# Kernel optimization log

Measured on AMD Instinct MI355X. Metric: run time of the kernel, lower is better.

Reference implementation:

```python
import jax, jax.numpy as jnp
import numpy as np

N = 100000   # nodes
D = 128      # in_ft == out_ft (residual mix requires equality)
E = 1600000  # edges (nnz of sparse A)


def setup_inputs() -> dict:
    key = jax.random.key(0)
    ks = jax.random.split(key, 8)
    X = jax.random.normal(ks[0], (N, D), dtype=jnp.float32)   # unused by forward math, kept for fidelity
    X0 = jax.random.normal(ks[1], (N, D), dtype=jnp.float32)
    row = jnp.sort(jax.random.randint(ks[2], (E,), 0, N))      # sparse A row indices (sorted)
    col = jax.random.randint(ks[3], (E,), 0, N)                # sparse A col indices
    vals = jax.random.uniform(ks[4], (E,), dtype=jnp.float32)  # sparse A values
    # nn.Linear(D, D): weight [out, in], bias [out]
    bound = 1.0 / np.sqrt(D)
    W = jax.random.uniform(ks[5], (D, D), minval=-bound, maxval=bound, dtype=jnp.float32)
    b = jax.random.uniform(ks[6], (D,), minval=-bound, maxval=bound, dtype=jnp.float32)
    alpha = jax.random.uniform(ks[7], (), dtype=jnp.float32)
    beta = jax.random.uniform(jax.random.fold_in(key, 7), (), dtype=jnp.float32)
    return {"X": X, "X0": X0, "row": row, "col": col, "vals": vals,
            "W": W, "b": b, "alpha": alpha, "beta": beta}


def reference(X, X0, row, col, vals, W, b, alpha, beta):
    # SpMM: (A @ X0)[i] = sum_e vals[e] * X0[col[e]] for edges with row[e] == i
    AX0 = jax.ops.segment_sum(vals[:, None] * X0[col], row, num_segments=N)  # [N, D]
    Xi = (1.0 - alpha) * AX0 + alpha * X0
    out = (1.0 - beta) * Xi + beta * (Xi @ W.T + b)
    return out
```

## Files before the change

### kernel.cpp

```cpp
#include <hip/hip_runtime.h>

#define D_FT 128

__device__ inline unsigned f2bf(float f) {
    unsigned u = __float_as_uint(f);
    return (u + 0x7FFFu + ((u >> 16) & 1u)) >> 16;
}
__device__ inline unsigned pack2bf(float a, float b) {
    return f2bf(a) | (f2bf(b) << 16);
}

typedef __attribute__((ext_vector_type(4))) float f32x4;
typedef __attribute__((ext_vector_type(8))) short bf16x8;

union bf8u { bf16x8 v; unsigned u[4]; };

__global__ __launch_bounds__(256) void build_row_ptr_kernel(
    const int* __restrict__ row, int* __restrict__ ptr, int n_edges, int n_nodes)
{
    const int e = blockIdx.x * 256 + threadIdx.x;
    if (e > n_edges) return;
    const int lo = (e == 0) ? 0 : row[e - 1] + 1;
    const int hi = (e == n_edges) ? n_nodes : row[e];
    for (int i = lo; i <= hi; ++i) ptr[i] = e;
}

template<bool USE_PTR>
__global__ __launch_bounds__(256) void spmm_mix_kernel(
    const float* __restrict__ X0,
    const int*   __restrict__ row,
    const int*   __restrict__ col,
    const float* __restrict__ vals,
    const int*   __restrict__ row_ptr,
    const float* __restrict__ alpha_p,
    float*       __restrict__ Xi,
    int n_nodes, int n_edges)
{
    const int wave = threadIdx.x >> 6;
    const int lane = threadIdx.x & 63;
    const int node = blockIdx.x * 4 + wave;
    if (node >= n_nodes) return;

    int ebeg, eend;
    if (USE_PTR) {
        ebeg = row_ptr[node];
        eend = row_ptr[node + 1];
    } else {
        int lo0 = 0, hi0 = n_edges, lo1 = 0, hi1 = n_edges;
        while ((lo0 < hi0) || (lo1 < hi1)) {
            int m0 = (lo0 + hi0) >> 1; if (m0 >= n_edges) m0 = n_edges - 1;
            int m1 = (lo1 + hi1) >> 1; if (m1 >= n_edges) m1 = n_edges - 1;
            const int r0v = row[m0];
            const int r1v = row[m1];
            if (lo0 < hi0) { if (r0v < node)     lo0 = m0 + 1; else hi0 = m0; }
            if (lo1 < hi1) { if (r1v < node + 1) lo1 = m1 + 1; else hi1 = m1; }
        }
        ebeg = lo0; eend = lo1;
    }

    const int d0 = lane * 2;
    float ax = 0.f, ay = 0.f;

    for (int e = ebeg; e < eend; e += 64) {
        const int n = min(64, eend - e);
        int   cl = 0; float vl = 0.f;
        if (lane < n) { cl = col[e + lane]; vl = vals[e + lane]; }
        for (int j0 = 0; j0 < n; j0 += 16) {
            float2 xs[16]; float vv[16];
            #pragma unroll
            for (int j = 0; j < 16; ++j) {
                const int c = __shfl(cl, j0 + j);
                vv[j] = __shfl(vl, j0 + j);
                xs[j] = *(const float2*)(X0 + (size_t)c * D_FT + d0);
            }
            #pragma unroll
            for (int j = 0; j < 16; ++j) {
                ax += vv[j] * xs[j].x;
                ay += vv[j] * xs[j].y;
            }
        }
    }

    const float alpha = *alpha_p;
    const float2 x0self = *(const float2*)(X0 + (size_t)node * D_FT + d0);
    float2 xi;
    xi.x = (1.f - alpha) * ax + alpha * x0self.x;
    xi.y = (1.f - alpha) * ay + alpha * x0self.y;
    *(float2*)(Xi + (size_t)node * D_FT + d0) = xi;
}

__global__ __launch_bounds__(256) void gemm_mix_kernel(
    const float* __restrict__ W,
    const float* __restrict__ bias,
    const float* __restrict__ beta_p,
    float*       __restrict__ io,
    int n_nodes)
{
    __shared__ __align__(16) char lds_raw[32768];
    char*  __restrict__ ldsB = lds_raw;
    float* __restrict__ ldsS = (float*)lds_raw;

    const int t   = threadIdx.x;
    const int w   = t >> 6;
    const int l   = t & 63;
    const int lhi = l >> 4;
    const int llo = l & 15;
    const int r0  = blockIdx.x * 64;

    int arow = r0 + w * 16 + llo;
    if (arow >= n_nodes) arow = n_nodes - 1;
    const float* aptr = io + (size_t)arow * D_FT;
    float4 af0[4], af1[4];
    #pragma unroll
    for (int ks = 0; ks < 4; ++ks) {
        const int k0 = ks * 32 + lhi * 8;
        af0[ks] = *(const float4*)(aptr + k0);
        af1[ks] = *(const float4*)(aptr + k0 + 4);
    }

    #pragma unroll
    for (int i = 0; i < 16; ++i) {
        const int f4 = i * 256 + t;
        const int o  = f4 >> 5;
        const int c4 = f4 & 31;
        const float4 x = *(const float4*)(W + (size_t)o * D_FT + c4 * 4);
        uint2 v; v.x = pack2bf(x.x, x.y); v.y = pack2bf(x.z, x.w);
        int byte = o * 256 + c4 * 8;
        byte ^= (o & 7) << 4;
        *(uint2*)(ldsB + byte) = v;
    }
    __syncthreads();

    f32x4 acc[8];
    #pragma unroll
    for (int n = 0; n < 8; ++n) acc[n] = (f32x4){0.f, 0.f, 0.f, 0.f};

    #pragma unroll
    for (int ks = 0; ks < 4; ++ks) {
        bf8u a;
        a.u[0] = pack2bf(af0[ks].x, af0[ks].y);
        a.u[1] = pack2bf(af0[ks].z, af0[ks].w);
        a.u[2] = pack2bf(af1[ks].x, af1[ks].y);
        a.u[3] = pack2bf(af1[ks].z, af1[ks].w);
        const int kb = ks * 64 + lhi * 16;
        #pragma unroll
        for (int n = 0; n < 8; ++n) {
            const int o = n * 16 + llo;
            int byte = o * 256 + kb;
            byte ^= (o & 7) << 4;
            const bf16x8 b = *(const bf16x8*)(ldsB + byte);
            acc[n] = __builtin_amdgcn_mfma_f32_16x16x32_bf16(a.v, b, acc[n], 0, 0, 0);
        }
    }

    __syncthreads();
    #pragma unroll
    for (int n = 0; n < 8; ++n) {
        const int C = n * 16 + llo;
        const int rt = w * 16 + lhi * 4;
        #pragma unroll
        for (int q = 0; q < 4; ++q)
            ldsS[(rt + q) * 128 + C] = acc[n][q];
    }
    __syncthreads();

    const float beta = *beta_p;
    const float ob = 1.f - beta;
    const int c4 = t & 31;
    const int rb = t >> 5;
    const float4 bb = *(const float4*)(bias + c4 * 4);

    #pragma unroll
    for (int i = 0; i < 8; ++i) {
        const int r  = rb * 8 + i;
        const int gr = r0 + r;
        if (gr < n_nodes) {
            const float4 a4  = *(const float4*)(ldsS + r * 128 + c4 * 4);
            const float4 xi4 = *(const float4*)(io + (size_t)gr * D_FT + c4 * 4);
            float4 o;
            o.x = ob * xi4.x + beta * (a4.x + bb.x);
            o.y = ob * xi4.y + beta * (a4.y + bb.y);
            o.z = ob * xi4.z + beta * (a4.z + bb.z);
            o.w = ob * xi4.w + beta * (a4.w + bb.w);
            *(float4*)(io + (size_t)gr * D_FT + c4 * 4) = o;
        }
    }
}

extern "C" void kernel_launch(void* const* d_in, const int* in_sizes, int n_in,
                              void* d_out, int out_size, void* d_ws, size_t ws_size,
                              hipStream_t stream) {
    const float* X0    = (const float*)d_in[1];
    const int*   row   = (const int*)  d_in[2];
    const int*   col   = (const int*)  d_in[3];
    const float* vals  = (const float*)d_in[4];
    const float* W     = (const float*)d_in[5];
    const float* b     = (const float*)d_in[6];
    const float* alpha = (const float*)d_in[7];
    const float* beta  = (const float*)d_in[8];
    float* out = (float*)d_out;

    const int n_nodes = in_sizes[1] / D_FT;
    const int n_edges = in_sizes[2];

    const size_t ptr_bytes = (size_t)(n_nodes + 1) * sizeof(int);
    const bool use_ptr = (ws_size >= ptr_bytes);

    if (use_ptr) {
        int* row_ptr = (int*)d_ws;
        build_row_ptr_kernel<<<(n_edges + 256) / 256, 256, 0, stream>>>(
            row, row_ptr, n_edges, n_nodes);
        spmm_mix_kernel<true><<<(n_nodes + 3) / 4, 256, 0, stream>>>(
            X0, row, col, vals, row_ptr, alpha, out, n_nodes, n_edges);
    } else {
        spmm_mix_kernel<false><<<(n_nodes + 3) / 4, 256, 0, stream>>>(
            X0, row, col, vals, nullptr, alpha, out, n_nodes, n_edges);
    }
    gemm_mix_kernel<<<(n_nodes + 63) / 64, 256, 0, stream>>>(
        W, b, beta, out, n_nodes);
}
```

Before: 274.9 us.

## Gather X0 in bf16 and pass bf16 intermediate from SpMM to GEMM

Adds a pre-pass that converts X0 to bf16 in workspace, so the SpMM gather reads 4 bytes per lane instead of 8 per edge row. The SpMM writes Xi as bf16 into workspace, and the GEMM reads the bf16 rows directly as MFMA A-fragments and writes fp32 output. This roughly halves the random-gather traffic and the intermediate traffic, at the cost of an extra conversion kernel and bf16 rounding of the aggregated features and of the residual term. Which path runs is selected by workspace size, with fp32 fallbacks kept.

```diff
diff --git a/kernel.cpp b/kernel.cpp
--- a/kernel.cpp
+++ b/kernel.cpp
@@ -9,11 +9,22 @@
 __device__ inline unsigned pack2bf(float a, float b) {
     return f2bf(a) | (f2bf(b) << 16);
 }
+__device__ inline float bf_lo(unsigned u) { return __uint_as_float(u << 16); }
+__device__ inline float bf_hi(unsigned u) { return __uint_as_float(u & 0xFFFF0000u); }
 
 typedef __attribute__((ext_vector_type(4))) float f32x4;
 typedef __attribute__((ext_vector_type(8))) short bf16x8;
 
-union bf8u { bf16x8 v; unsigned u[4]; };
+__global__ __launch_bounds__(256) void convert_x0_kernel(
+    const float* __restrict__ X0, unsigned* __restrict__ xb, int n4)
+{
+    const int i = blockIdx.x * 256 + threadIdx.x;
+    if (i < n4) {
+        const float4 x = ((const float4*)X0)[i];
+        uint2 v; v.x = pack2bf(x.x, x.y); v.y = pack2bf(x.z, x.w);
+        ((uint2*)xb)[i] = v;
+    }
+}
 
 __global__ __launch_bounds__(256) void build_row_ptr_kernel(
     const int* __restrict__ row, int* __restrict__ ptr, int n_edges, int n_nodes)
@@ -25,15 +36,17 @@
     for (int i = lo; i <= hi; ++i) ptr[i] = e;
 }
 
-template<bool USE_PTR>
+template<bool GB, bool XB, bool PTR>
 __global__ __launch_bounds__(256) void spmm_mix_kernel(
-    const float* __restrict__ X0,
-    const int*   __restrict__ row,
-    const int*   __restrict__ col,
-    const float* __restrict__ vals,
-    const int*   __restrict__ row_ptr,
-    const float* __restrict__ alpha_p,
-    float*       __restrict__ Xi,
+    const float*    __restrict__ X0,
+    const unsigned* __restrict__ X0b,
+    const int*      __restrict__ row,
+    const int*      __restrict__ col,
+    const float*    __restrict__ vals,
+    const int*      __restrict__ row_ptr,
+    const float*    __restrict__ alpha_p,
+    float*          __restrict__ Xi_f32,
+    unsigned*       __restrict__ Xi_bf,
     int n_nodes, int n_edges)
 {
     const int wave = threadIdx.x >> 6;
@@ -42,7 +55,7 @@
     if (node >= n_nodes) return;
 
     int ebeg, eend;
-    if (USE_PTR) {
+    if (PTR) {
         ebeg = row_ptr[node];
         eend = row_ptr[node + 1];
     } else {
@@ -66,17 +79,33 @@
         int   cl = 0; float vl = 0.f;
         if (lane < n) { cl = col[e + lane]; vl = vals[e + lane]; }
         for (int j0 = 0; j0 < n; j0 += 16) {
-            float2 xs[16]; float vv[16];
-            #pragma unroll
-            for (int j = 0; j < 16; ++j) {
-                const int c = __shfl(cl, j0 + j);
-                vv[j] = __shfl(vl, j0 + j);
-                xs[j] = *(const float2*)(X0 + (size_t)c * D_FT + d0);
-            }
-            #pragma unroll
-            for (int j = 0; j < 16; ++j) {
-                ax += vv[j] * xs[j].x;
-                ay += vv[j] * xs[j].y;
+            float vv[16];
+            if (GB) {
+                unsigned xs[16];
+                #pragma unroll
+                for (int j = 0; j < 16; ++j) {
+                    const int c = __shfl(cl, j0 + j);
+                    vv[j] = __shfl(vl, j0 + j);
+                    xs[j] = X0b[c * 64 + lane];
+                }
+                #pragma unroll
+                for (int j = 0; j < 16; ++j) {
+                    ax += vv[j] * bf_lo(xs[j]);
+                    ay += vv[j] * bf_hi(xs[j]);
+                }
+            } else {
+                float2 xs[16];
+                #pragma unroll
+                for (int j = 0; j < 16; ++j) {
+                    const int c = __shfl(cl, j0 + j);
+                    vv[j] = __shfl(vl, j0 + j);
+                    xs[j] = *(const float2*)(X0 + (size_t)c * D_FT + d0);
+                }
+                #pragma unroll
+                for (int j = 0; j < 16; ++j) {
+                    ax += vv[j] * xs[j].x;
+                    ay += vv[j] * xs[j].y;
+                }
             }
         }
     }
@@ -86,10 +115,107 @@
     float2 xi;
     xi.x = (1.f - alpha) * ax + alpha * x0self.x;
     xi.y = (1.f - alpha) * ay + alpha * x0self.y;
-    *(float2*)(Xi + (size_t)node * D_FT + d0) = xi;
-}
-
-__global__ __launch_bounds__(256) void gemm_mix_kernel(
+    if (XB) {
+        Xi_bf[node * 64 + lane] = pack2bf(xi.x, xi.y);
+    } else {
+        *(float2*)(Xi_f32 + (size_t)node * D_FT + d0) = xi;
+    }
+}
+
+__global__ __launch_bounds__(256) void gemm_mix_bf16_kernel(
+    const float*    __restrict__ W,
+    const float*    __restrict__ bias,
+    const float*    __restrict__ beta_p,
+    const unsigned* __restrict__ xi,
+    float*          __restrict__ out,
+    int n_nodes)
+{
+    __shared__ __align__(16) char lds_raw[32768];
+    char*  __restrict__ ldsB = lds_raw;
+    float* __restrict__ ldsS = (float*)lds_raw;
+
+    const int t   = threadIdx.x;
+    const int w   = t >> 6;
+    const int l   = t & 63;
+    const int lhi = l >> 4;
+    const int llo = l & 15;
+    const int r0  = blockIdx.x * 64;
+
+    int arow = r0 + w * 16 + llo;
+    if (arow >= n_nodes) arow = n_nodes - 1;
+    const char* aptr = (const char*)xi + (size_t)arow * 256;
+    bf16x8 a[4];
+    #pragma unroll
+    for (int ks = 0; ks < 4; ++ks)
+        a[ks] = *(const bf16x8*)(aptr + ks * 64 + lhi * 16);
+
+    #pragma unroll
+    for (int i = 0; i < 16; ++i) {
+        const int f4 = i * 256 + t;
+        const int o  = f4 >> 5;
+        const int c4 = f4 & 31;
+        const float4 x = *(const float4*)(W + (size_t)o * D_FT + c4 * 4);
+        uint2 v; v.x = pack2bf(x.x, x.y); v.y = pack2bf(x.z, x.w);
+        int byte = o * 256 + c4 * 8;
+        byte ^= (o & 7) << 4;
+        *(uint2*)(ldsB + byte) = v;
+    }
+    __syncthreads();
+
+    f32x4 acc[8];
+    #pragma unroll
+    for (int n = 0; n < 8; ++n) acc[n] = (f32x4){0.f, 0.f, 0.f, 0.f};
+
+    #pragma unroll
+    for (int ks = 0; ks < 4; ++ks) {
+        const int kb = ks * 64 + lhi * 16;
+        #pragma unroll
+        for (int n = 0; n < 8; ++n) {
+            const int o = n * 16 + llo;
+            int byte = o * 256 + kb;
+            byte ^= (o & 7) << 4;
+            const bf16x8 b = *(const bf16x8*)(ldsB + byte);
+            acc[n] = __builtin_amdgcn_mfma_f32_16x16x32_bf16(a[ks], b, acc[n], 0, 0, 0);
+        }
+    }
+
+    __syncthreads();
+    #pragma unroll
+    for (int n = 0; n < 8; ++n) {
+        const int C = n * 16 + llo;
+        const int rt = w * 16 + lhi * 4;
+        #pragma unroll
+        for (int q = 0; q < 4; ++q)
+            ldsS[(rt + q) * 128 + C] = acc[n][q];
+    }
+    __syncthreads();
+
+    const float beta = *beta_p;
+    const float ob = 1.f - beta;
+    const int c4 = t & 31;
+    const int rb = t >> 5;
+    const float4 bb = *(const float4*)(bias + c4 * 4);
+
+    #pragma unroll
+    for (int i = 0; i < 8; ++i) {
+        const int r  = rb * 8 + i;
+        const int gr = r0 + r;
+        if (gr < n_nodes) {
+            const float4 a4 = *(const float4*)(ldsS + r * 128 + c4 * 4);
+            const uint2  p  = ((const uint2*)(xi + (size_t)gr * 64))[c4];
+            float4 o;
+            o.x = ob * bf_lo(p.x) + beta * (a4.x + bb.x);
+            o.y = ob * bf_hi(p.x) + beta * (a4.y + bb.y);
+            o.z = ob * bf_lo(p.y) + beta * (a4.z + bb.z);
+            o.w = ob * bf_hi(p.y) + beta * (a4.w + bb.w);
+            *(float4*)(out + (size_t)gr * D_FT + c4 * 4) = o;
+        }
+    }
+}
+
+union bf8u { bf16x8 v; unsigned u[4]; };
+
+__global__ __launch_bounds__(256) void gemm_mix_f32_kernel(
     const float* __restrict__ W,
     const float* __restrict__ bias,
     const float* __restrict__ beta_p,
@@ -204,18 +330,47 @@
     const int n_edges = in_sizes[2];
 
     const size_t ptr_bytes = (size_t)(n_nodes + 1) * sizeof(int);
-    const bool use_ptr = (ws_size >= ptr_bytes);
-
-    if (use_ptr) {
-        int* row_ptr = (int*)d_ws;
+    const size_t BFOFF  = 524288;
+    const size_t BFSZ   = (size_t)n_nodes * 256;
+    const bool ptr_ok = (ws_size >= ptr_bytes);
+    const bool tierA  = ptr_ok && (ws_size >= BFOFF + 2 * BFSZ);
+    const bool tierAp = !tierA && ptr_ok && (ws_size >= BFOFF + BFSZ);
+
+    int* row_ptr = (int*)d_ws;
+    if (ptr_ok)
         build_row_ptr_kernel<<<(n_edges + 256) / 256, 256, 0, stream>>>(
             row, row_ptr, n_edges, n_nodes);
-        spmm_mix_kernel<true><<<(n_nodes + 3) / 4, 256, 0, stream>>>(
-            X0, row, col, vals, row_ptr, alpha, out, n_nodes, n_edges);
+
+    const int spmm_grid = (n_nodes + 3) / 4;
+
+    if (tierA) {
+        unsigned* X0b  = (unsigned*)((char*)d_ws + BFOFF);
+        unsigned* Xibf = (unsigned*)((char*)d_ws + BFOFF + BFSZ);
+        const int n4 = n_nodes * D_FT / 4;
+        convert_x0_kernel<<<(n4 + 255) / 256, 256, 0, stream>>>(X0, X0b, n4);
+        spmm_mix_kernel<true, true, true><<<spmm_grid, 256, 0, stream>>>(
+            X0, X0b, row, col, vals, row_ptr, alpha, nullptr, Xibf,
+            n_nodes, n_edges);
+        gemm_mix_bf16_kernel<<<(n_nodes + 63) / 64, 256, 0, stream>>>(
+            W, b, beta, Xibf, out, n_nodes);
+    } else if (tierAp) {
+        unsigned* Xibf = (unsigned*)((char*)d_ws + BFOFF);
+        spmm_mix_kernel<false, true, true><<<spmm_grid, 256, 0, stream>>>(
+            X0, nullptr, row, col, vals, row_ptr, alpha, nullptr, Xibf,
+            n_nodes, n_edges);
+        gemm_mix_bf16_kernel<<<(n_nodes + 63) / 64, 256, 0, stream>>>(
+            W, b, beta, Xibf, out, n_nodes);
+    } else if (ptr_ok) {
+        spmm_mix_kernel<false, false, true><<<spmm_grid, 256, 0, stream>>>(
+            X0, nullptr, row, col, vals, row_ptr, alpha, out, nullptr,
+            n_nodes, n_edges);
+        gemm_mix_f32_kernel<<<(n_nodes + 63) / 64, 256, 0, stream>>>(
+            W, b, beta, out, n_nodes);
     } else {
-        spmm_mix_kernel<false><<<(n_nodes + 3) / 4, 256, 0, stream>>>(
-            X0, row, col, vals, nullptr, alpha, out, n_nodes, n_edges);
-    }
-    gemm_mix_kernel<<<(n_nodes + 63) / 64, 256, 0, stream>>>(
-        W, b, beta, out, n_nodes);
-}
+        spmm_mix_kernel<false, false, false><<<spmm_grid, 256, 0, stream>>>(
+            X0, nullptr, row, col, vals, nullptr, alpha, out, nullptr,
+            n_nodes, n_edges);
+        gemm_mix_f32_kernel<<<(n_nodes + 63) / 64, 256, 0, stream>>>(
+            W, b, beta, out, n_nodes);
+    }
+}
```

Measured after the change: 242.8 us. 1.13x faster.

## Fuse SpMM and GEMM via LDS and gather from a bf16 copy of X0

Applied to the files above, without the earlier changes.

Adds a pre-pass that converts X0 to bf16 in workspace, halving the bytes of each random row gather in SpMM. Each block of 512 threads now computes Xi for 128 nodes into LDS as bf16, then runs the MFMA GEMM and the beta mix directly, so the Xi round trip through global memory is gone. The costs are an extra conversion kernel, lower precision for the gathered X0 and for the residual Xi, uncoalesced scalar output stores, and lower occupancy from 64KB of LDS. The fused path needs a large enough workspace and falls back to the old path otherwise.

```diff
diff --git a/kernel.cpp b/kernel.cpp
--- a/kernel.cpp
+++ b/kernel.cpp
@@ -9,11 +9,24 @@
 __device__ inline unsigned pack2bf(float a, float b) {
     return f2bf(a) | (f2bf(b) << 16);
 }
+__device__ inline float bf_lo(unsigned u) { return __uint_as_float(u << 16); }
+__device__ inline float bf_hi(unsigned u) { return __uint_as_float(u & 0xFFFF0000u); }
+__device__ inline float bf_us(unsigned short u) { return __uint_as_float((unsigned)u << 16); }
 
 typedef __attribute__((ext_vector_type(4))) float f32x4;
 typedef __attribute__((ext_vector_type(8))) short bf16x8;
-
 union bf8u { bf16x8 v; unsigned u[4]; };
+
+__global__ __launch_bounds__(256) void convert_x0_kernel(
+    const float* __restrict__ X0, unsigned* __restrict__ xb, int n4)
+{
+    const int i = blockIdx.x * 256 + threadIdx.x;
+    if (i < n4) {
+        const float4 x = ((const float4*)X0)[i];
+        uint2 v; v.x = pack2bf(x.x, x.y); v.y = pack2bf(x.z, x.w);
+        ((uint2*)xb)[i] = v;
+    }
+}
 
 __global__ __launch_bounds__(256) void build_row_ptr_kernel(
     const int* __restrict__ row, int* __restrict__ ptr, int n_edges, int n_nodes)
@@ -25,7 +38,130 @@
     for (int i = lo; i <= hi; ++i) ptr[i] = e;
 }
 
-template<bool USE_PTR>
+__global__ __launch_bounds__(512) void fused_spmm_gemm_kernel(
+    const unsigned* __restrict__ X0b,
+    const int*      __restrict__ col,
+    const float*    __restrict__ vals,
+    const int*      __restrict__ row_ptr,
+    const float*    __restrict__ W,
+    const float*    __restrict__ bias,
+    const float*    __restrict__ alpha_p,
+    const float*    __restrict__ beta_p,
+    float*          __restrict__ out,
+    int n_nodes)
+{
+    __shared__ __align__(16) char lds_raw[65536];
+    char* __restrict__ ldsXi = lds_raw;
+    char* __restrict__ ldsW  = lds_raw + 32768;
+
+    const int t    = threadIdx.x;
+    const int wid  = t >> 6;
+    const int lane = t & 63;
+    const int bn   = blockIdx.x * 128;
+    const float alpha = *alpha_p;
+
+    for (int i = 0; i < 16; ++i) {
+        const int nl   = wid * 16 + i;
+        const int node = bn + nl;
+        unsigned xw = 0;
+        if (node < n_nodes) {
+            const int ebeg = row_ptr[node];
+            const int eend = row_ptr[node + 1];
+            float ax = 0.f, ay = 0.f;
+            for (int e = ebeg; e < eend; e += 64) {
+                const int n = min(64, eend - e);
+                int cl = 0; float vl = 0.f;
+                if (lane < n) { cl = col[e + lane]; vl = vals[e + lane]; }
+                for (int j0 = 0; j0 < n; j0 += 16) {
+                    float vv[16]; unsigned xs[16];
+                    #pragma unroll
+                    for (int j = 0; j < 16; ++j) {
+                        const int c = __shfl(cl, j0 + j);
+                        vv[j] = __shfl(vl, j0 + j);
+                        xs[j] = X0b[c * 64 + lane];
+                    }
+                    #pragma unroll
+                    for (int j = 0; j < 16; ++j) {
+                        ax += vv[j] * bf_lo(xs[j]);
+                        ay += vv[j] * bf_hi(xs[j]);
+                    }
+                }
+            }
+            const unsigned s = X0b[node * 64 + lane];
+            xw = pack2bf((1.f - alpha) * ax + alpha * bf_lo(s),
+                         (1.f - alpha) * ay + alpha * bf_hi(s));
+        }
+        int byte = nl * 256 + lane * 4;
+        byte ^= (nl & 7) << 4;
+        *(unsigned*)(ldsXi + byte) = xw;
+    }
+
+    #pragma unroll
+    for (int i = 0; i < 8; ++i) {
+        const int f4 = i * 512 + t;
+        const int o  = f4 >> 5;
+        const int c4 = f4 & 31;
+        const float4 x = *(const float4*)(W + (size_t)o * D_FT + c4 * 4);
+        uint2 v; v.x = pack2bf(x.x, x.y); v.y = pack2bf(x.z, x.w);
+        int byte = o * 256 + c4 * 8;
+        byte ^= (o & 7) << 4;
+        *(uint2*)(ldsW + byte) = v;
+    }
+    __syncthreads();
+
+    const int llo = lane & 15;
+    const int lhi = lane >> 4;
+
+    bf16x8 a[4];
+    #pragma unroll
+    for (int ks = 0; ks < 4; ++ks) {
+        const int r = wid * 16 + llo;
+        int byte = r * 256 + ks * 64 + lhi * 16;
+        byte ^= (r & 7) << 4;
+        a[ks] = *(const bf16x8*)(ldsXi + byte);
+    }
+
+    f32x4 acc[8];
+    #pragma unroll
+    for (int n = 0; n < 8; ++n) acc[n] = (f32x4){0.f, 0.f, 0.f, 0.f};
+
+    #pragma unroll
+    for (int ks = 0; ks < 4; ++ks) {
+        const int kb = ks * 64 + lhi * 16;
+        #pragma unroll
+        for (int n = 0; n < 8; ++n) {
+            const int o = n * 16 + llo;
+            int byte = o * 256 + kb;
+            byte ^= (o & 7) << 4;
+            const bf16x8 b = *(const bf16x8*)(ldsW + byte);
+            acc[n] = __builtin_amdgcn_mfma_f32_16x16x32_bf16(a[ks], b, acc[n], 0, 0, 0);
+        }
+    }
+
+    const float beta = *beta_p;
+    const float ob = 1.f - beta;
+    float bb[8];
+    #pragma unroll
+    for (int n = 0; n < 8; ++n) bb[n] = bias[n * 16 + llo];
+
+    #pragma unroll
+    for (int q = 0; q < 4; ++q) {
+        const int rl = wid * 16 + lhi * 4 + q;
+        const int R  = bn + rl;
+        if (R < n_nodes) {
+            #pragma unroll
+            for (int n = 0; n < 8; ++n) {
+                const int C = n * 16 + llo;
+                int byte = rl * 256 + C * 2;
+                byte ^= (rl & 7) << 4;
+                const float xi = bf_us(*(const unsigned short*)(ldsXi + byte));
+                out[(size_t)R * D_FT + C] = ob * xi + beta * (acc[n][q] + bb[n]);
+            }
+        }
+    }
+}
+
+template<bool PTR>
 __global__ __launch_bounds__(256) void spmm_mix_kernel(
     const float* __restrict__ X0,
     const int*   __restrict__ row,
@@ -42,7 +178,7 @@
     if (node >= n_nodes) return;
 
     int ebeg, eend;
-    if (USE_PTR) {
+    if (PTR) {
         ebeg = row_ptr[node];
         eend = row_ptr[node + 1];
     } else {
@@ -63,7 +199,7 @@
 
     for (int e = ebeg; e < eend; e += 64) {
         const int n = min(64, eend - e);
-        int   cl = 0; float vl = 0.f;
+        int cl = 0; float vl = 0.f;
         if (lane < n) { cl = col[e + lane]; vl = vals[e + lane]; }
         for (int j0 = 0; j0 < n; j0 += 16) {
             float2 xs[16]; float vv[16];
@@ -89,7 +225,7 @@
     *(float2*)(Xi + (size_t)node * D_FT + d0) = xi;
 }
 
-__global__ __launch_bounds__(256) void gemm_mix_kernel(
+__global__ __launch_bounds__(256) void gemm_mix_f32_kernel(
     const float* __restrict__ W,
     const float* __restrict__ bias,
     const float* __restrict__ beta_p,
@@ -204,18 +340,32 @@
     const int n_edges = in_sizes[2];
 
     const size_t ptr_bytes = (size_t)(n_nodes + 1) * sizeof(int);
-    const bool use_ptr = (ws_size >= ptr_bytes);
-
-    if (use_ptr) {
+    const size_t BFOFF = 524288;
+    const size_t BFSZ  = (size_t)n_nodes * 256;
+    const bool ptr_ok = (ws_size >= ptr_bytes);
+    const bool fused  = ptr_ok && (ws_size >= BFOFF + BFSZ) && (BFOFF >= ptr_bytes);
+
+    if (fused) {
+        int*      row_ptr = (int*)d_ws;
+        unsigned* X0b     = (unsigned*)((char*)d_ws + BFOFF);
+        build_row_ptr_kernel<<<(n_edges + 256) / 256, 256, 0, stream>>>(
+            row, row_ptr, n_edges, n_nodes);
+        const int n4 = n_nodes * D_FT / 4;
+        convert_x0_kernel<<<(n4 + 255) / 256, 256, 0, stream>>>(X0, X0b, n4);
+        fused_spmm_gemm_kernel<<<(n_nodes + 127) / 128, 512, 0, stream>>>(
+            X0b, col, vals, row_ptr, W, b, alpha, beta, out, n_nodes);
+    } else if (ptr_ok) {
         int* row_ptr = (int*)d_ws;
         build_row_ptr_kernel<<<(n_edges + 256) / 256, 256, 0, stream>>>(
             row, row_ptr, n_edges, n_nodes);
         spmm_mix_kernel<true><<<(n_nodes + 3) / 4, 256, 0, stream>>>(
             X0, row, col, vals, row_ptr, alpha, out, n_nodes, n_edges);
+        gemm_mix_f32_kernel<<<(n_nodes + 63) / 64, 256, 0, stream>>>(
+            W, b, beta, out, n_nodes);
     } else {
         spmm_mix_kernel<false><<<(n_nodes + 3) / 4, 256, 0, stream>>>(
             X0, row, col, vals, nullptr, alpha, out, n_nodes, n_edges);
-    }
-    gemm_mix_kernel<<<(n_nodes + 63) / 64, 256, 0, stream>>>(
-        W, b, beta, out, n_nodes);
-}
+        gemm_mix_f32_kernel<<<(n_nodes + 63) / 64, 256, 0, stream>>>(
+            W, b, beta, out, n_nodes);
+    }
+}
```

After: 252.2 us. -8.2%, faster.
